# Performance work log

Measured on AMD Instinct MI355X. Metric: run time of the kernel, lower is better.

Reference implementation:

```python
import jax, jax.numpy as jnp
import numpy as np

N_NODES = 100000
N_EDGES = 1600000


def _degrees(src, dst, n):
    ones = jnp.ones(src.shape[0], dtype=jnp.float32)
    deg_out = jax.ops.segment_sum(ones, src, num_segments=n)
    deg_in = jax.ops.segment_sum(ones, dst, num_segments=n)
    out_norm = jnp.where(deg_out > 0, jax.lax.rsqrt(jnp.maximum(deg_out, 1.0)), 0.0)
    in_norm = jnp.where(deg_in > 0, jax.lax.rsqrt(jnp.maximum(deg_in, 1.0)), 0.0)
    return out_norm, in_norm


def _graph_conv(h, W, b, src, dst, out_norm, in_norm, act):
    # DGL GraphConv, norm='both': D_out^{-1/2} on src, aggregate, D_in^{-1/2} on dst
    h = h * out_norm[:, None]
    h = h @ W  # project first (in >= out) to shrink edge traffic
    msg = h[src]  # [E, d] gather
    agg = jax.ops.segment_sum(msg, dst, num_segments=h.shape[0])
    agg = agg * in_norm[:, None] + b
    return act(agg) if act is not None else agg


def setup_inputs() -> dict:
    key = jax.random.key(0)
    ks = jax.random.split(key, 8)
    feats = jax.random.normal(ks[0], (N_NODES, 512), dtype=jnp.float32)
    src = jax.random.randint(ks[1], (N_EDGES,), 0, N_NODES)
    dst = jax.random.randint(ks[2], (N_EDGES,), 0, N_NODES)
    W0 = jax.random.normal(ks[3], (512, 256), dtype=jnp.float32) * 0.05
    b0 = jnp.zeros((256,), dtype=jnp.float32)
    Ws = jax.random.normal(ks[4], (5, 256, 256), dtype=jnp.float32) * 0.05
    bs = jnp.zeros((5, 256), dtype=jnp.float32)
    W_out = jax.random.normal(ks[5], (256, 40), dtype=jnp.float32) * 0.05
    b_out = jnp.zeros((40,), dtype=jnp.float32)
    return {"features": feats, "src": src, "dst": dst, "W0": W0, "b0": b0,
            "Ws": Ws, "bs": bs, "W_out": W_out, "b_out": b_out}


def reference(features, src, dst, W0, b0, Ws, bs, W_out, b_out):
    out_norm, in_norm = _degrees(src, dst, features.shape[0])
    act = jax.nn.relu
    # layer 0
    h = _graph_conv(features, W0, b0, src, dst, out_norm, in_norm, act)
    jk = h  # running max over layer outputs (JK max-pool)
    # layers 1..5 (dropout is identity in eval mode)
    for i in range(Ws.shape[0]):
        h = _graph_conv(h, Ws[i], bs[i], src, dst, out_norm, in_norm, act)
        jk = jnp.maximum(jk, h)
    # final GraphConv (no activation) on JK-pooled features, then log_softmax
    h = _graph_conv(jk, W_out, b_out, src, dst, out_norm, in_norm, None)
    return jax.nn.log_softmax(h, axis=1)
```

## Files before the change

kernel.cpp:

```cpp
#include <hip/hip_runtime.h>
#include <hip/hip_bf16.h>
#include <math.h>

#define N_NODES 100000
#define N_EDGES 1600000
#define SCAN_B 1024
#define SCAN_NB ((N_NODES + SCAN_B - 1) / SCAN_B)

typedef _Float16 f16;
typedef f16 f16x8 __attribute__((ext_vector_type(8)));
typedef float f32x4 __attribute__((ext_vector_type(4)));
typedef unsigned short u16;
typedef u16 u16x8 __attribute__((ext_vector_type(8)));
typedef u16 u16x4 __attribute__((ext_vector_type(4)));

__device__ __forceinline__ u16 f16bits(float f) {
  union { f16 h; u16 u; } c; c.h = (f16)f; return c.u;
}
__device__ __forceinline__ float f16val(u16 b) {
  union { u16 u; f16 h; } c; c.u = b; return (float)c.h;
}

__device__ __forceinline__ void gload16(const void* g, void* l) {
  __builtin_amdgcn_global_load_lds(
      (const __attribute__((address_space(1))) void*)g,
      (__attribute__((address_space(3))) void*)l, 16, 0, 0);
}


__global__ void k_count(const int* __restrict__ src, const int* __restrict__ dst,
                        int* __restrict__ deg_out, int* __restrict__ deg_in) {
  int i = blockIdx.x * blockDim.x + threadIdx.x;
  int stride = gridDim.x * blockDim.x;
  for (; i < N_EDGES; i += stride) {
    atomicAdd(&deg_out[src[i]], 1);
    atomicAdd(&deg_in[dst[i]], 1);
  }
}

__global__ void k_norms(const int* __restrict__ deg_out, const int* __restrict__ deg_in,
                        float* __restrict__ norm_out, float* __restrict__ norm_in) {
  int i = blockIdx.x * blockDim.x + threadIdx.x;
  if (i < N_NODES) {
    int a = deg_out[i], b = deg_in[i];
    norm_out[i] = a > 0 ? rsqrtf((float)a) : 0.f;
    norm_in[i]  = b > 0 ? rsqrtf((float)b) : 0.f;
  }
}

__global__ __launch_bounds__(1024) void k_scan1(const int* __restrict__ deg,
                                                int* __restrict__ bsum) {
  __shared__ int red[16];
  int b = blockIdx.x, t = threadIdx.x;
  int i = b * SCAN_B + t;
  int x = (i < N_NODES) ? deg[i] : 0;
#pragma unroll
  for (int o = 32; o > 0; o >>= 1) x += __shfl_down(x, o, 64);
  if ((t & 63) == 0) red[t >> 6] = x;
  __syncthreads();
  if (t == 0) {
    int s = 0;
#pragma unroll
    for (int j = 0; j < 16; ++j) s += red[j];
    bsum[b] = s;
  }
}

__global__ __launch_bounds__(128) void k_scan2(const int* __restrict__ bsum,
                                               int* __restrict__ boffs) {
  __shared__ int buf[128];
  int t = threadIdx.x;
  int x = (t < SCAN_NB) ? bsum[t] : 0;
  buf[t] = x;
  __syncthreads();
  for (int off = 1; off < 128; off <<= 1) {
    int v = (t >= off) ? buf[t - off] : 0;
    __syncthreads();
    buf[t] += v;
    __syncthreads();
  }
  if (t < SCAN_NB) boffs[t] = (t > 0) ? buf[t - 1] : 0;
}

__global__ __launch_bounds__(1024) void k_scan3(const int* __restrict__ deg,
                                                const int* __restrict__ boffs,
                                                int* __restrict__ row_ptr) {
  __shared__ int buf[SCAN_B];
  int b = blockIdx.x, t = threadIdx.x;
  int i = b * SCAN_B + t;
  int x = (i < N_NODES) ? deg[i] : 0;
  buf[t] = x;
  __syncthreads();
  for (int off = 1; off < SCAN_B; off <<= 1) {
    int v = (t >= off) ? buf[t - off] : 0;
    __syncthreads();
    buf[t] += v;
    __syncthreads();
  }
  if (i < N_NODES) row_ptr[i + 1] = boffs[b] + buf[t];
  if (i == 0) row_ptr[0] = 0;
}

__global__ void k_fill(const int* __restrict__ src, const int* __restrict__ dst,
                       const int* __restrict__ row_ptr, int* __restrict__ cursor,
                       int* __restrict__ csr_src) {
  int i = blockIdx.x * blockDim.x + threadIdx.x;
  int stride = gridDim.x * blockDim.x;
  for (; i < N_EDGES; i += stride) {
    int d = dst[i];
    int p = atomicAdd(&cursor[d], 1);
    csr_src[row_ptr[d] + p] = src[i];
  }
}

__global__ void k_wconv(const float* __restrict__ W, int K, int N, int NB,
                        u16* __restrict__ Wt) {
  int i = blockIdx.x * blockDim.x + threadIdx.x;
  if (i >= NB * K) return;
  int col = i / K, k = i - col * K;
  float v = (col < N) ? W[(size_t)k * N + col] : 0.f;
  Wt[i] = f16bits(v);
}


template <int NBCOL, int OUTF32>
__global__ __launch_bounds__(256) void k_gemm_p(
    const u16* __restrict__ Ax, int K,
    const u16* __restrict__ Bx,
    void* __restrict__ Cv, int ldc, int M, int Ncols, int NBrow) {
  __shared__ u16 sA[2][8][4][16][8];
  __shared__ u16 sB[2][8][4][16][8];

  int p = blockIdx.x;
  int row, col;
  if (NBCOL == 2) {
    int nb = NBrow * 2;
    int cut = (nb >> 4) << 4;
    if (p < cut) { row = ((p >> 4) << 3) + (p & 7); col = (p >> 3) & 1; }
    else { int q = p - cut; row = (cut >> 1) + (q >> 1); col = q & 1; }
  } else { row = p; col = 0; }
  int rowBase = row * 128;
  int colBase = col * 128;

  int t = threadIdx.x;
  int w = t >> 6, l = t & 63;
  int lr = l & 15;
  int kc = l >> 4;

  int gaR0 = min(rowBase + w * 16 + lr, M - 1);
  int gaR1 = min(rowBase + (4 + w) * 16 + lr, M - 1);
  int gbR0 = colBase + w * 16 + lr;
  int gbR1 = colBase + (4 + w) * 16 + lr;

  const u16* pA0 = Ax + (size_t)gaR0 * K + kc * 8;
  const u16* pA1 = Ax + (size_t)gaR1 * K + kc * 8;
  const u16* pB0 = Bx + (size_t)gbR0 * K + kc * 8;
  const u16* pB1 = Bx + (size_t)gbR1 * K + kc * 8;

  int wr = (w >> 1) * 64, wc = (w & 1) * 64;
  int rbA = (w >> 1) * 4;
  int rbB = (w & 1) * 4;
  int crow = kc * 4;

  f32x4 acc[4][4];
#pragma unroll
  for (int r = 0; r < 4; ++r)
#pragma unroll
    for (int c = 0; c < 4; ++c) acc[r][c] = (f32x4)(0.f);

  auto stage = [&](int bb, int k0) {
    gload16(pA0 + k0, &sA[bb][w][0][0][0]);
    gload16(pA1 + k0, &sA[bb][4 + w][0][0][0]);
    gload16(pB0 + k0, &sB[bb][w][0][0][0]);
    gload16(pB1 + k0, &sB[bb][4 + w][0][0][0]);
  };

  int NS = K >> 5;
  stage(0, 0);
  for (int s = 0; s < NS; ++s) {
    int bb = s & 1;
    if (s + 1 < NS) {
      stage(bb ^ 1, (s + 1) * 32);
      asm volatile("s_waitcnt vmcnt(4)" ::: "memory");
    } else {
      asm volatile("s_waitcnt vmcnt(0)" ::: "memory");
    }
    __builtin_amdgcn_s_barrier();

    f16x8 a[4], b[4];
#pragma unroll
    for (int r = 0; r < 4; ++r) a[r] = *(const f16x8*)&sA[bb][rbA + r][kc][lr][0];
#pragma unroll
    for (int c = 0; c < 4; ++c) b[c] = *(const f16x8*)&sB[bb][rbB + c][kc][lr][0];
#pragma unroll
    for (int r = 0; r < 4; ++r)
#pragma unroll
      for (int c = 0; c < 4; ++c)
        acc[r][c] = __builtin_amdgcn_mfma_f32_16x16x32_f16(a[r], b[c], acc[r][c], 0, 0, 0);

    __builtin_amdgcn_s_barrier();
  }

#pragma unroll
  for (int r = 0; r < 4; ++r)
#pragma unroll
    for (int c = 0; c < 4; ++c) {
      int ccol = colBase + wc + c * 16 + lr;
      if (ccol < Ncols) {
#pragma unroll
        for (int j = 0; j < 4; ++j) {
          int rrow = rowBase + wr + r * 16 + crow + j;
          if (rrow < M) {
            if (OUTF32) ((float*)Cv)[(size_t)rrow * ldc + ccol] = acc[r][c][j];
            else        ((u16*)Cv)[(size_t)rrow * ldc + ccol] = f16bits(acc[r][c][j]);
          }
        }
      }
    }
}


__global__ __launch_bounds__(256) void k_gemm_l0(
    const float* __restrict__ Af, int K,
    const u16* __restrict__ Bx,
    const float* __restrict__ rowscale,
    u16* __restrict__ C, int ldc, int M, int Ncols) {
  __shared__ u16 sA[8][4][16][8];
  __shared__ u16 sB[8][4][16][8];

  int t = threadIdx.x;
  int colBase = blockIdx.x * 128;
  int rowBase = blockIdx.y * 128;

  int w = t >> 6, l = t & 63;
  int lr = l & 15;
  int kc = l >> 4;

  int gaR0 = min(rowBase + w * 16 + lr, M - 1);
  int gaR1 = min(rowBase + (4 + w) * 16 + lr, M - 1);
  int gbR0 = colBase + w * 16 + lr;
  int gbR1 = colBase + (4 + w) * 16 + lr;

  float rs0 = rowscale[gaR0], rs1 = rowscale[gaR1];

  int wr = (w >> 1) * 64, wc = (w & 1) * 64;
  int rbA = (w >> 1) * 4;
  int rbB = (w & 1) * 4;
  int crow = kc * 4;

  f32x4 acc[4][4];
#pragma unroll
  for (int r = 0; r < 4; ++r)
#pragma unroll
    for (int c = 0; c < 4; ++c) acc[r][c] = (f32x4)(0.f);

  for (int k0 = 0; k0 < K; k0 += 32) {
    __syncthreads();
    {
      const float* p0 = Af + (size_t)gaR0 * K + k0 + kc * 8;
      const float* p1 = Af + (size_t)gaR1 * K + k0 + kc * 8;
      float4 v0 = *(const float4*)p0;
      float4 v1 = *(const float4*)(p0 + 4);
      u16x8 h;
      h[0] = f16bits(v0.x * rs0); h[1] = f16bits(v0.y * rs0);
      h[2] = f16bits(v0.z * rs0); h[3] = f16bits(v0.w * rs0);
      h[4] = f16bits(v1.x * rs0); h[5] = f16bits(v1.y * rs0);
      h[6] = f16bits(v1.z * rs0); h[7] = f16bits(v1.w * rs0);
      *(u16x8*)&sA[w][kc][lr][0] = h;
      float4 w0 = *(const float4*)p1;
      float4 w1 = *(const float4*)(p1 + 4);
      h[0] = f16bits(w0.x * rs1); h[1] = f16bits(w0.y * rs1);
      h[2] = f16bits(w0.z * rs1); h[3] = f16bits(w0.w * rs1);
      h[4] = f16bits(w1.x * rs1); h[5] = f16bits(w1.y * rs1);
      h[6] = f16bits(w1.z * rs1); h[7] = f16bits(w1.w * rs1);
      *(u16x8*)&sA[4 + w][kc][lr][0] = h;
    }
    gload16(Bx + (size_t)gbR0 * K + k0 + kc * 8, &sB[w][0][0][0]);
    gload16(Bx + (size_t)gbR1 * K + k0 + kc * 8, &sB[4 + w][0][0][0]);
    __syncthreads();

    f16x8 a[4], b[4];
#pragma unroll
    for (int r = 0; r < 4; ++r) a[r] = *(const f16x8*)&sA[rbA + r][kc][lr][0];
#pragma unroll
    for (int c = 0; c < 4; ++c) b[c] = *(const f16x8*)&sB[rbB + c][kc][lr][0];
#pragma unroll
    for (int r = 0; r < 4; ++r)
#pragma unroll
      for (int c = 0; c < 4; ++c)
        acc[r][c] = __builtin_amdgcn_mfma_f32_16x16x32_f16(a[r], b[c], acc[r][c], 0, 0, 0);
  }

#pragma unroll
  for (int r = 0; r < 4; ++r)
#pragma unroll
    for (int c = 0; c < 4; ++c) {
      int col = colBase + wc + c * 16 + lr;
      if (col < Ncols) {
#pragma unroll
        for (int j = 0; j < 4; ++j) {
          int row = rowBase + wr + r * 16 + crow + j;
          if (row < M) C[(size_t)row * ldc + col] = f16bits(acc[r][c][j]);
        }
      }
    }
}


__global__ __launch_bounds__(256) void k_agg(const u16* __restrict__ proj,
                                             const int* __restrict__ row_ptr,
                                             const int* __restrict__ csr_src,
                                             const float* __restrict__ norm_in,
                                             const float* __restrict__ norm_out,
                                             const float* __restrict__ bias,
                                             u16* __restrict__ hF,
                                             u16* __restrict__ jk, int mode) {
  int wid = __builtin_amdgcn_readfirstlane(threadIdx.x >> 6);
  int node = blockIdx.x * 4 + wid;
  if (node >= N_NODES) return;
  int l4 = (threadIdx.x & 63) * 4;

  int s = row_ptr[node], e = row_ptr[node + 1];
  f32x4 a0 = (f32x4)(0.f), a1 = (f32x4)(0.f), a2 = (f32x4)(0.f), a3 = (f32x4)(0.f);
  int i = s;
  for (; i + 7 < e; i += 8) {
    int u0 = csr_src[i + 0], u1 = csr_src[i + 1], u2 = csr_src[i + 2], u3 = csr_src[i + 3];
    int u4 = csr_src[i + 4], u5 = csr_src[i + 5], u6 = csr_src[i + 6], u7 = csr_src[i + 7];
    u16x4 r0 = *(const u16x4*)(proj + (size_t)u0 * 256 + l4);
    u16x4 r1 = *(const u16x4*)(proj + (size_t)u1 * 256 + l4);
    u16x4 r2 = *(const u16x4*)(proj + (size_t)u2 * 256 + l4);
    u16x4 r3 = *(const u16x4*)(proj + (size_t)u3 * 256 + l4);
    u16x4 r4 = *(const u16x4*)(proj + (size_t)u4 * 256 + l4);
    u16x4 r5 = *(const u16x4*)(proj + (size_t)u5 * 256 + l4);
    u16x4 r6 = *(const u16x4*)(proj + (size_t)u6 * 256 + l4);
    u16x4 r7 = *(const u16x4*)(proj + (size_t)u7 * 256 + l4);
#pragma unroll
    for (int j = 0; j < 4; ++j) {
      a0[j] += f16val(r0[j]) + f16val(r4[j]);
      a1[j] += f16val(r1[j]) + f16val(r5[j]);
      a2[j] += f16val(r2[j]) + f16val(r6[j]);
      a3[j] += f16val(r3[j]) + f16val(r7[j]);
    }
  }
  for (; i + 3 < e; i += 4) {
    int u0 = csr_src[i + 0], u1 = csr_src[i + 1], u2 = csr_src[i + 2], u3 = csr_src[i + 3];
    u16x4 r0 = *(const u16x4*)(proj + (size_t)u0 * 256 + l4);
    u16x4 r1 = *(const u16x4*)(proj + (size_t)u1 * 256 + l4);
    u16x4 r2 = *(const u16x4*)(proj + (size_t)u2 * 256 + l4);
    u16x4 r3 = *(const u16x4*)(proj + (size_t)u3 * 256 + l4);
#pragma unroll
    for (int j = 0; j < 4; ++j) {
      a0[j] += f16val(r0[j]);
      a1[j] += f16val(r1[j]);
      a2[j] += f16val(r2[j]);
      a3[j] += f16val(r3[j]);
    }
  }
  for (; i < e; ++i) {
    u16x4 r0 = *(const u16x4*)(proj + (size_t)csr_src[i] * 256 + l4);
#pragma unroll
    for (int j = 0; j < 4; ++j) a0[j] += f16val(r0[j]);
  }

  float nin = norm_in[node];
  f32x4 b4 = *(const f32x4*)(bias + l4);
  f32x4 v = ((a0 + a1) + (a2 + a3)) * nin + b4;
#pragma unroll
  for (int j = 0; j < 4; ++j) v[j] = fmaxf(v[j], 0.f);

  size_t idx = (size_t)node * 256 + l4;
  f32x4 pv = v;
  if (mode == 0) {
    u16x4 jw;
#pragma unroll
    for (int j = 0; j < 4; ++j) jw[j] = f16bits(v[j]);
    *(u16x4*)(jk + idx) = jw;
  } else {
    u16x4 jold = *(const u16x4*)(jk + idx);
    f32x4 jv;
#pragma unroll
    for (int j = 0; j < 4; ++j) jv[j] = fmaxf(f16val(jold[j]), v[j]);
    if (mode == 1) {
      u16x4 jw;
#pragma unroll
      for (int j = 0; j < 4; ++j) jw[j] = f16bits(jv[j]);
      *(u16x4*)(jk + idx) = jw;
    } else {
      pv = jv;
    }
  }

  float nout = norm_out[node];
  u16x4 hw;
#pragma unroll
  for (int j = 0; j < 4; ++j) hw[j] = f16bits(pv[j] * nout);
  *(u16x4*)(hF + idx) = hw;
}


__global__ __launch_bounds__(64) void k_agg_out(const u16* __restrict__ proj,
                                                const int* __restrict__ row_ptr,
                                                const int* __restrict__ csr_src,
                                                const float* __restrict__ norm_in,
                                                const float* __restrict__ b_out,
                                                float* __restrict__ out) {
  int n = blockIdx.x;
  int c = threadIdx.x;
  int s = row_ptr[n], e = row_ptr[n + 1];
  float a0 = 0.f, a1 = 0.f, a2 = 0.f, a3 = 0.f;
  int i = s;
  for (; i + 3 < e; i += 4) {
    a0 += f16val(proj[(size_t)csr_src[i] * 64 + c]);
    a1 += f16val(proj[(size_t)csr_src[i + 1] * 64 + c]);
    a2 += f16val(proj[(size_t)csr_src[i + 2] * 64 + c]);
    a3 += f16val(proj[(size_t)csr_src[i + 3] * 64 + c]);
  }
  for (; i < e; ++i) a0 += f16val(proj[(size_t)csr_src[i] * 64 + c]);
  float acc = (a0 + a1) + (a2 + a3);
  float v = acc * norm_in[n] + ((c < 40) ? b_out[c] : 0.f);
  float vm = (c < 40) ? v : -3.0e38f;
  float m = vm;
#pragma unroll
  for (int o = 32; o > 0; o >>= 1) m = fmaxf(m, __shfl_xor(m, o, 64));
  float ex = (c < 40) ? __expf(v - m) : 0.f;
  float ssum = ex;
#pragma unroll
  for (int o = 32; o > 0; o >>= 1) ssum += __shfl_xor(ssum, o, 64);
  float lse = m + logf(ssum);
  if (c < 40) out[(size_t)n * 40 + c] = v - lse;
}


extern "C" void kernel_launch(void* const* d_in, const int* in_sizes, int n_in,
                              void* d_out, int out_size, void* d_ws, size_t ws_size,
                              hipStream_t stream) {
  const float* feats = (const float*)d_in[0];
  const int*   src   = (const int*)d_in[1];
  const int*   dst   = (const int*)d_in[2];
  const float* W0    = (const float*)d_in[3];
  const float* b0    = (const float*)d_in[4];
  const float* Ws    = (const float*)d_in[5];
  const float* bs    = (const float*)d_in[6];
  const float* W_out = (const float*)d_in[7];
  const float* b_out = (const float*)d_in[8];
  float* out = (float*)d_out;

  char* base = (char*)d_ws;
  size_t off = 0;
  auto alloc = [&](size_t bytes) -> void* {
    off = (off + 255) & ~(size_t)255;
    void* r = base + off;
    off += bytes;
    return r;
  };
  float* norm_out = (float*)alloc((size_t)N_NODES * 4);
  float* norm_in  = (float*)alloc((size_t)N_NODES * 4);
  int*   deg_out  = (int*)alloc((size_t)N_NODES * 4);
  int*   deg_in   = (int*)alloc((size_t)N_NODES * 4);
  int*   cursor   = (int*)alloc((size_t)N_NODES * 4);
  int*   row_ptr  = (int*)alloc((size_t)(N_NODES + 1) * 4);
  int*   bsum     = (int*)alloc((size_t)SCAN_NB * 4);
  int*   boffs    = (int*)alloc((size_t)SCAN_NB * 4);
  int*   csr_src  = (int*)alloc((size_t)N_EDGES * 4);
  u16*   Wt0      = (u16*)alloc((size_t)256 * 512 * 2);
  u16*   Wts      = (u16*)alloc((size_t)5 * 256 * 256 * 2);
  u16*   Wto      = (u16*)alloc((size_t)128 * 256 * 2);
  u16*   proj40   = (u16*)alloc((size_t)N_NODES * 64 * 2);
  u16*   hF       = (u16*)alloc((size_t)N_NODES * 256 * 2);
  u16*   bufC     = (u16*)alloc((size_t)N_NODES * 256 * 2);
  u16*   jk       = (u16*)alloc((size_t)N_NODES * 256 * 2);
  (void)ws_size; (void)in_sizes; (void)n_in; (void)out_size;

  hipMemsetAsync(deg_out, 0, (size_t)N_NODES * 4, stream);
  hipMemsetAsync(deg_in,  0, (size_t)N_NODES * 4, stream);
  hipMemsetAsync(cursor,  0, (size_t)N_NODES * 4, stream);

  k_count<<<2048, 256, 0, stream>>>(src, dst, deg_out, deg_in);
  k_norms<<<(N_NODES + 255) / 256, 256, 0, stream>>>(deg_out, deg_in, norm_out, norm_in);
  k_scan1<<<SCAN_NB, 1024, 0, stream>>>(deg_in, bsum);
  k_scan2<<<1, 128, 0, stream>>>(bsum, boffs);
  k_scan3<<<SCAN_NB, 1024, 0, stream>>>(deg_in, boffs, row_ptr);
  k_fill<<<2048, 256, 0, stream>>>(src, dst, row_ptr, cursor, csr_src);

  k_wconv<<<(256 * 512 + 255) / 256, 256, 0, stream>>>(W0, 512, 256, 256, Wt0);
  for (int ll = 0; ll < 5; ++ll)
    k_wconv<<<(256 * 256 + 255) / 256, 256, 0, stream>>>(
        Ws + (size_t)ll * 256 * 256, 256, 256, 256, Wts + (size_t)ll * 256 * 256);
  k_wconv<<<(128 * 256 + 255) / 256, 256, 0, stream>>>(W_out, 256, 40, 128, Wto);

  const int NBROW = (N_NODES + 127) / 128;
  dim3 ga((N_NODES + 3) / 4);
  k_gemm_l0<<<dim3(2, NBROW), 256, 0, stream>>>(feats, 512, Wt0,
                                                norm_out, bufC, 256, N_NODES, 256);
  k_agg<<<ga, 256, 0, stream>>>(bufC, row_ptr, csr_src, norm_in, norm_out, b0,
                                hF, jk, 0);
  for (int ll = 0; ll < 5; ++ll) {
    k_gemm_p<2, 0><<<NBROW * 2, 256, 0, stream>>>(hF, 256,
                                                  Wts + (size_t)ll * 256 * 256,
                                                  bufC, 256, N_NODES, 256, NBROW);
    int mode = (ll == 4) ? 2 : 1;
    const float* bias = bs + (size_t)ll * 256;
    k_agg<<<ga, 256, 0, stream>>>(bufC, row_ptr, csr_src, norm_in, norm_out, bias,
                                  hF, jk, mode);
  }
  k_gemm_p<1, 0><<<NBROW, 256, 0, stream>>>(hF, 256, Wto,
                                            proj40, 64, N_NODES, 64, NBROW);
  k_agg_out<<<N_NODES, 64, 0, stream>>>(proj40, row_ptr, csr_src, norm_in, b_out, out);
}
```

Measured before the change: 1.406 ms.

## Build CSR via two-pass bucketing by destination block for locality

Replaces the single random-scatter CSR fill with two passes. The first scatters (src,dst) pairs into coarse buckets of 128 destination nodes. The second has one block per bucket place edges into their final CSR slots, so the atomics and writes stay within a small address range. This aims to cut scattered atomic and write traffic, at the cost of an extra 12.8MB pairs buffer being written and read plus one more kernel launch.

```diff
diff --git a/kernel.cpp b/kernel.cpp
--- a/kernel.cpp
+++ b/kernel.cpp
@@ -6,6 +6,8 @@
 #define N_EDGES 1600000
 #define SCAN_B 1024
 #define SCAN_NB ((N_NODES + SCAN_B - 1) / SCAN_B)
+#define BKT_SH 7
+#define NBKT ((N_NODES + 127) >> 7)
 
 typedef _Float16 f16;
 typedef f16 f16x8 __attribute__((ext_vector_type(8)));
@@ -101,15 +103,32 @@
   if (i == 0) row_ptr[0] = 0;
 }
 
-__global__ void k_fill(const int* __restrict__ src, const int* __restrict__ dst,
-                       const int* __restrict__ row_ptr, int* __restrict__ cursor,
-                       int* __restrict__ csr_src) {
+
+__global__ void k_bucket(const int* __restrict__ src, const int* __restrict__ dst,
+                         const int* __restrict__ row_ptr,
+                         int* __restrict__ bkt_cur, int2* __restrict__ pairs) {
   int i = blockIdx.x * blockDim.x + threadIdx.x;
   int stride = gridDim.x * blockDim.x;
   for (; i < N_EDGES; i += stride) {
-    int d = dst[i];
-    int p = atomicAdd(&cursor[d], 1);
-    csr_src[row_ptr[d] + p] = src[i];
+    int s = src[i], d = dst[i];
+    int b = d >> BKT_SH;
+    int p = atomicAdd(&bkt_cur[b], 1);
+    pairs[row_ptr[b << BKT_SH] + p] = make_int2(s, d);
+  }
+}
+
+
+__global__ __launch_bounds__(256) void k_fill2(const int2* __restrict__ pairs,
+                                               const int* __restrict__ row_ptr,
+                                               int* __restrict__ cursor,
+                                               int* __restrict__ csr_src) {
+  int b = blockIdx.x;
+  int lo = row_ptr[b << BKT_SH];
+  int hi = row_ptr[min((b + 1) << BKT_SH, N_NODES)];
+  for (int i = lo + threadIdx.x; i < hi; i += 256) {
+    int2 e = pairs[i];
+    int p = atomicAdd(&cursor[e.y], 1);
+    csr_src[row_ptr[e.y] + p] = e.x;
   }
 }
 
@@ -461,7 +480,9 @@
   int*   row_ptr  = (int*)alloc((size_t)(N_NODES + 1) * 4);
   int*   bsum     = (int*)alloc((size_t)SCAN_NB * 4);
   int*   boffs    = (int*)alloc((size_t)SCAN_NB * 4);
+  int*   bkt_cur  = (int*)alloc((size_t)NBKT * 4);
   int*   csr_src  = (int*)alloc((size_t)N_EDGES * 4);
+  int2*  pairs    = (int2*)alloc((size_t)N_EDGES * 8);
   u16*   Wt0      = (u16*)alloc((size_t)256 * 512 * 2);
   u16*   Wts      = (u16*)alloc((size_t)5 * 256 * 256 * 2);
   u16*   Wto      = (u16*)alloc((size_t)128 * 256 * 2);
@@ -474,13 +495,15 @@
   hipMemsetAsync(deg_out, 0, (size_t)N_NODES * 4, stream);
   hipMemsetAsync(deg_in,  0, (size_t)N_NODES * 4, stream);
   hipMemsetAsync(cursor,  0, (size_t)N_NODES * 4, stream);
+  hipMemsetAsync(bkt_cur, 0, (size_t)NBKT * 4, stream);
 
   k_count<<<2048, 256, 0, stream>>>(src, dst, deg_out, deg_in);
   k_norms<<<(N_NODES + 255) / 256, 256, 0, stream>>>(deg_out, deg_in, norm_out, norm_in);
   k_scan1<<<SCAN_NB, 1024, 0, stream>>>(deg_in, bsum);
   k_scan2<<<1, 128, 0, stream>>>(bsum, boffs);
   k_scan3<<<SCAN_NB, 1024, 0, stream>>>(deg_in, boffs, row_ptr);
-  k_fill<<<2048, 256, 0, stream>>>(src, dst, row_ptr, cursor, csr_src);
+  k_bucket<<<2048, 256, 0, stream>>>(src, dst, row_ptr, bkt_cur, pairs);
+  k_fill2<<<NBKT, 256, 0, stream>>>(pairs, row_ptr, cursor, csr_src);
 
   k_wconv<<<(256 * 512 + 255) / 256, 256, 0, stream>>>(W0, 512, 256, 256, Wt0);
   for (int ll = 0; ll < 5; ++ll)
```

Result: slower. 1.728 ms (+22.9%).
